# Performance work log

Measured on AMD Instinct MI355X. Metric: run time of the kernel, lower is better.

The kernel has to match this reference:

```python
import jax, jax.numpy as jnp
import numpy as np
import math

D_INNER = 512
D_STATE = 16
DT_RANK = 32
B_SZ = 2
L_SEQ = 4096


def setup_inputs() -> dict:
    key = jax.random.key(0)
    ks = jax.random.split(key, 6)
    x = jax.random.normal(ks[0], (B_SZ, L_SEQ, D_INNER), dtype=jnp.float32)
    # parameters (match torch init semantics closely enough for a numeric baseline)
    A = jnp.arange(1, D_STATE + 1, dtype=jnp.float32)
    A_log = jnp.broadcast_to(jnp.log(A)[None, :], (D_INNER, D_STATE)).copy()
    D_param = jnp.ones((D_INNER,), dtype=jnp.float32)
    # x_proj: Linear(d_inner -> dt_rank + 2*d_state), no bias
    W_xproj = jax.random.normal(ks[1], (DT_RANK + 2 * D_STATE, D_INNER), dtype=jnp.float32) / np.sqrt(D_INNER)
    # dt_proj: Linear(dt_rank -> d_inner) with special bias init
    W_dt = jax.random.normal(ks[2], (D_INNER, DT_RANK), dtype=jnp.float32) / np.sqrt(DT_RANK)
    dt_init = jnp.exp(jax.random.uniform(ks[3], (D_INNER,)) * (math.log(0.1) - math.log(0.001)) + math.log(0.001))
    b_dt = jnp.log(jnp.exp(dt_init) - 1.0)
    alpha = jnp.asarray(0.6, dtype=jnp.float32)
    beta_logit = jnp.asarray(math.log(0.99 / (1.0 - 0.99 + 1e-08)), dtype=jnp.float32)
    return {"x": x, "A_log": A_log, "D_param": D_param, "W_xproj": W_xproj,
            "W_dt": W_dt, "b_dt": b_dt, "alpha": alpha, "beta_logit": beta_logit}


def _momentum_ssm(x, A_log, D_param, W_xproj, W_dt, b_dt, alpha, beta_logit):
    # x: (B, L, D)
    proj = jnp.einsum('bld,pd->blp', x, W_xproj)            # (B, L, r+2N)
    dt_in = proj[..., :DT_RANK]
    Bp = proj[..., DT_RANK:DT_RANK + D_STATE]                # (B, L, N)
    Cp = proj[..., DT_RANK + D_STATE:]                       # (B, L, N)
    dt = jax.nn.softplus(jnp.einsum('blr,dr->bld', dt_in, W_dt) + b_dt)  # (B, L, D)
    A = -jnp.exp(A_log)                                      # (D, N)
    A_bar = jnp.exp(dt[..., None] * A[None, None])           # (B, L, D, N)
    # fused B_bar * x_t: dt * Bp * x
    inp = dt[..., None] * Bp[:, :, None, :] * x[..., None]   # (B, L, D, N)
    beta = jax.nn.sigmoid(beta_logit)

    # scan over time; carry (h, v): (B, D, N)
    h0 = jnp.zeros((x.shape[0], D_INNER, D_STATE), dtype=x.dtype)
    v0 = jnp.zeros_like(h0)

    def step(carry, ts):
        h, v = carry
        a_t, inp_t, c_t = ts                                 # (B,D,N), (B,D,N), (B,N)
        v = beta * v + alpha * inp_t
        h = a_t * h + v
        y = jnp.einsum('bdn,bn->bd', h, c_t)
        return (h, v), y

    xs = (jnp.moveaxis(A_bar, 1, 0), jnp.moveaxis(inp, 1, 0), jnp.moveaxis(Cp, 1, 0))
    _, ys = jax.lax.scan(step, (h0, v0), xs)                 # ys: (L, B, D)
    y = jnp.moveaxis(ys, 0, 1)                               # (B, L, D)
    return y + D_param * x


def reference(x, A_log, D_param, W_xproj, W_dt, b_dt, alpha, beta_logit):
    return _momentum_ssm(x, A_log, D_param, W_xproj, W_dt, b_dt, alpha, beta_logit)
```

## Files before the change

kernel.cpp:

```cpp
#include <hip/hip_runtime.h>


#define D_IN 512
#define D_ST 16
#define DTR  32
#define BSZ  2
#define LSEQ 4096
#define PDIM 64
#define NCH  256
#define LCH  (LSEQ / NCH)
#define LOG2E 1.44269504f
#define LN2   0.69314718f

typedef __attribute__((ext_vector_type(8))) short short8;
typedef __attribute__((ext_vector_type(4))) float f32x4;
typedef _Float16 f16;
typedef __attribute__((ext_vector_type(8))) _Float16 f16x8;

__device__ inline float fast_exp2(float x) { return __builtin_amdgcn_exp2f(x); }
__device__ inline float fast_log2(float x) { return __builtin_amdgcn_logf(x); }

__device__ inline unsigned short bf16_rne(float f) {
  unsigned b = __float_as_uint(f);
  return (unsigned short)((b + 0x7fffu + ((b >> 16) & 1u)) >> 16);
}

__device__ inline void cvt8(const float4 u, const float4 v, short8& hi, short8& lo) {
  float f[8] = {u.x, u.y, u.z, u.w, v.x, v.y, v.z, v.w};
#pragma unroll
  for (int i = 0; i < 8; ++i) {
    unsigned short h = bf16_rne(f[i]);
    hi[i] = (short)h;
    float r = f[i] - __uint_as_float((unsigned)h << 16);
    lo[i] = (short)bf16_rne(r);
  }
}

__device__ inline void st16h(f16* p, const float* s) {
  f16 t[16];
#pragma unroll
  for (int i = 0; i < 16; ++i) t[i] = (f16)s[i];
  *(f16x8*)p = *(f16x8*)&t[0];
  *(f16x8*)(p + 8) = *(f16x8*)&t[8];
}
__device__ inline void ld16h(const f16* p, float* d) {
  f16x8 a = *(const f16x8*)p;
  f16x8 b = *(const f16x8*)(p + 8);
#pragma unroll
  for (int i = 0; i < 8; ++i) { d[i] = (float)a[i]; d[8 + i] = (float)b[i]; }
}

#define PWCHK(val, n)                                                        \
  pw = pw && (fabsf((val) - (float)((n) + 1) * a0) <=                        \
              2e-5f * fabsf((float)((n) + 1) * a0));

__device__ inline bool detectA2(const float* __restrict__ A_log, int d, float& a0) {
  const float4* ap = (const float4*)(A_log + (size_t)d * D_ST);
  float4 r0 = ap[0], r1 = ap[1], r2 = ap[2], r3 = ap[3];
  float4 e0 = make_float4(-__expf(r0.x) * LOG2E, -__expf(r0.y) * LOG2E,
                          -__expf(r0.z) * LOG2E, -__expf(r0.w) * LOG2E);
  float4 e1 = make_float4(-__expf(r1.x) * LOG2E, -__expf(r1.y) * LOG2E,
                          -__expf(r1.z) * LOG2E, -__expf(r1.w) * LOG2E);
  float4 e2 = make_float4(-__expf(r2.x) * LOG2E, -__expf(r2.y) * LOG2E,
                          -__expf(r2.z) * LOG2E, -__expf(r2.w) * LOG2E);
  float4 e3 = make_float4(-__expf(r3.x) * LOG2E, -__expf(r3.y) * LOG2E,
                          -__expf(r3.z) * LOG2E, -__expf(r3.w) * LOG2E);
  a0 = e0.x;
  bool pw = true;
  PWCHK(e0.y, 1) PWCHK(e0.z, 2) PWCHK(e0.w, 3)
  PWCHK(e1.x, 4) PWCHK(e1.y, 5) PWCHK(e1.z, 6) PWCHK(e1.w, 7)
  PWCHK(e2.x, 8) PWCHK(e2.y, 9) PWCHK(e2.z, 10) PWCHK(e2.w, 11)
  PWCHK(e3.x, 12) PWCHK(e3.y, 13) PWCHK(e3.z, 14) PWCHK(e3.w, 15)
  return pw;
}

#define MM3(ACC, AH, AL, BH, BL)                                        \
  ACC = __builtin_amdgcn_mfma_f32_16x16x32_bf16(AL, BH, ACC, 0, 0, 0);  \
  ACC = __builtin_amdgcn_mfma_f32_16x16x32_bf16(AH, BL, ACC, 0, 0, 0);  \
  ACC = __builtin_amdgcn_mfma_f32_16x16x32_bf16(AH, BH, ACC, 0, 0, 0);

#define LOADBF(P, S)                                          \
  {                                                           \
    const int kb = (S) * 32;                                  \
    float4 a0 = *(const float4*)(wr + kb);                    \
    float4 b0 = *(const float4*)(wr + kb + 4);                \
    float4 a1 = *(const float4*)(wr + 8192 + kb);             \
    float4 b1 = *(const float4*)(wr + 8192 + kb + 4);         \
    float4 a2 = *(const float4*)(wr + 16384 + kb);            \
    float4 b2 = *(const float4*)(wr + 16384 + kb + 4);        \
    float4 a3 = *(const float4*)(wr + 24576 + kb);            \
    float4 b3 = *(const float4*)(wr + 24576 + kb + 4);        \
    cvt8(a0, b0, P##h0, P##l0);                               \
    cvt8(a1, b1, P##h1, P##l1);                               \
    cvt8(a2, b2, P##h2, P##l2);                               \
    cvt8(a3, b3, P##h3, P##l3);                               \
  }

#define LOADA(Aa, Ab, S)                              \
  {                                                   \
    const int ka = (S) * 32;                          \
    Aa = *(const float4*)(xr + ka);                   \
    Ab = *(const float4*)(xr + ka + 4);               \
  }

#define COMPSTEP(Aa, Ab, P)                           \
  {                                                   \
    short8 ahi, alo;                                  \
    cvt8(Aa, Ab, ahi, alo);                           \
    MM3(acc0, ahi, alo, P##h0, P##l0);                \
    MM3(acc1, ahi, alo, P##h1, P##l1);                \
    MM3(acc2, ahi, alo, P##h2, P##l2);                \
    MM3(acc3, ahi, alo, P##h3, P##l3);                \
  }

__global__ __launch_bounds__(256) void k_proj(const float* __restrict__ x,
                                              const float* __restrict__ W,
                                              float* __restrict__ proj) {
  __shared__ float Pacc[4][16][64];
  const int row0 = blockIdx.x * 16;
  const int l = threadIdx.x & 63;
  const int wq = threadIdx.x >> 6;
  const int m = l & 15;
  const int ko = (l >> 4) * 8 + wq * 128;
  const float* xr = x + (size_t)(row0 + m) * D_IN + ko;
  const float* wr = W + (size_t)m * D_IN + ko;

  f32x4 acc0 = {0.f, 0.f, 0.f, 0.f}, acc1 = acc0, acc2 = acc0, acc3 = acc0;
  float4 A0a, A0b, A1a, A1b, A2a, A2b, A3a, A3b;
  short8 Xh0, Xh1, Xh2, Xh3, Xl0, Xl1, Xl2, Xl3;
  short8 Yh0, Yh1, Yh2, Yh3, Yl0, Yl1, Yl2, Yl3;
  LOADA(A0a, A0b, 0); LOADA(A1a, A1b, 1); LOADA(A2a, A2b, 2); LOADA(A3a, A3b, 3);
  LOADBF(X, 0); LOADBF(Y, 1);

  COMPSTEP(A0a, A0b, X); LOADBF(X, 2);
  COMPSTEP(A1a, A1b, Y); LOADBF(Y, 3);
  COMPSTEP(A2a, A2b, X);
  COMPSTEP(A3a, A3b, Y);

  const int r0 = (l >> 4) * 4;
#pragma unroll
  for (int r = 0; r < 4; ++r) {
    Pacc[wq][r0 + r][m] = acc0[r];
    Pacc[wq][r0 + r][16 + m] = acc1[r];
    Pacc[wq][r0 + r][32 + m] = acc2[r];
    Pacc[wq][r0 + r][48 + m] = acc3[r];
  }
  __syncthreads();

  const int orow = threadIdx.x >> 4;
  const int ocol = (threadIdx.x & 15) * 4;
  float4 s0 = *(const float4*)&Pacc[0][orow][ocol];
  float4 s1 = *(const float4*)&Pacc[1][orow][ocol];
  float4 s2 = *(const float4*)&Pacc[2][orow][ocol];
  float4 s3 = *(const float4*)&Pacc[3][orow][ocol];
  float4 o = make_float4((s0.x + s1.x) + (s2.x + s3.x), (s0.y + s1.y) + (s2.y + s3.y),
                         (s0.z + s1.z) + (s2.z + s3.z), (s0.w + s1.w) + (s2.w + s3.w));
  *(float4*)(proj + (size_t)(row0 + orow) * PDIM + ocol) = o;
}

#define S1_LOOP                                                              \
  _Pragma("unroll")                                                          \
  for (int j = 0; j < LCH; ++j) {                                            \
    const float4* pj = (const float4*)(pb + j * PDIM);                       \
    float4 pp[8];                                                            \
    _Pragma("unroll")                                                        \
    for (int k = 0; k < 8; ++k) pp[k] = pj[k];                               \
    float c0 = bb, c1 = 0.f, c2 = 0.f, c3 = 0.f;                             \
    _Pragma("unroll")                                                        \
    for (int k = 0; k < 8; ++k) {                                            \
      c0 = fmaf(pp[k].x, w4[k].x, c0);                                       \
      c1 = fmaf(pp[k].y, w4[k].y, c1);                                       \
      c2 = fmaf(pp[k].z, w4[k].z, c2);                                       \
      c3 = fmaf(pp[k].w, w4[k].w, c3);                                       \
    }                                                                        \
    const float acc = (c0 + c1) + (c2 + c3);                                 \
    const float ee = fast_exp2(acc * LOG2E);                                 \
    const float dtc = (acc > 20.f) ? acc : LN2 * fast_log2(1.f + ee);        \
    dp[(size_t)j * D_IN] = (f16)dtc;                                         \
    sd += dtc;                                                               \
    bpow *= beta;                                                            \
    const float u = alpha * dtc * xs[j];                                     \
    float4 bq[4];                                                            \
    _Pragma("unroll")                                                        \
    for (int k = 0; k < 4; ++k) bq[k] = pj[8 + k];                           \
    const float* Bf = (const float*)bq;                                      \
    AR_INIT;                                                                 \
    _Pragma("unroll")                                                        \
    for (int n = 0; n < 16; ++n) {                                           \
      AR_STEP;                                                               \
      v[n] = fmaf(beta, v[n], u * Bf[n]);                                    \
      h[n] = fmaf(ar, h[n], v[n]);                                           \
      cv[n] = fmaf(ar, cv[n], bpow);                                         \
    }                                                                        \
  }

__global__ __launch_bounds__(256) void k_scan1(const float* __restrict__ x,
                                               const float* __restrict__ proj,
                                               const float* __restrict__ A_log,
                                               const float* __restrict__ W_dt,
                                               const float* __restrict__ b_dt,
                                               const float* __restrict__ alpha_p,
                                               const float* __restrict__ beta_p,
                                               f16* __restrict__ hh,
                                               f16* __restrict__ vh,
                                               f16* __restrict__ cvv,
                                               float* __restrict__ sdt,
                                               f16* __restrict__ dth) {
  const int c = blockIdx.x, b = blockIdx.z;
  const int d = blockIdx.y * 256 + threadIdx.x;
  const int t0 = c * LCH;
  const float* pb = proj + ((size_t)b * LSEQ + t0) * PDIM;

  float xs[LCH];
  {
    const float* xp = x + ((size_t)b * LSEQ + t0) * D_IN + d;
#pragma unroll
    for (int j = 0; j < LCH; ++j) xs[j] = xp[(size_t)j * D_IN];
  }
  float4 w4[8];
  {
    const float4* wp = (const float4*)(W_dt + (size_t)d * DTR);
#pragma unroll
    for (int i = 0; i < 8; ++i) w4[i] = wp[i];
  }
  const float bb = b_dt[d];
  const float alpha = alpha_p[0];
  const float beta = 1.f / (1.f + __expf(-beta_p[0]));
  float a0;
  const bool pw = detectA2(A_log, d, a0);

  f16* dp = dth + ((size_t)b * LSEQ + t0) * D_IN + d;
  float h[16] = {}, v[16] = {}, cv[16] = {};
  float bpow = 1.f, sd = 0.f;

  if (pw) {
#define AR_INIT const float r = fast_exp2(dtc * a0); float ar = 1.f
#define AR_STEP ar *= r
    S1_LOOP
#undef AR_INIT
#undef AR_STEP
  } else {
    volatile const float* av = A_log + (size_t)d * D_ST;
#define AR_INIT float ar
#define AR_STEP ar = fast_exp2(dtc * (-__expf(av[n]) * LOG2E))
    S1_LOOP
#undef AR_INIT
#undef AR_STEP
  }

  const size_t base = ((size_t)(b * NCH + c) * D_IN + d) * D_ST;
  st16h(hh + base, h);
  st16h(vh + base, v);
  st16h(cvv + base, cv);
  sdt[(size_t)(b * NCH + c) * D_IN + d] = sd;
}

__global__ __launch_bounds__(1024) void k_fix(f16* __restrict__ hh,
                                              f16* __restrict__ vh,
                                              const f16* __restrict__ cvv,
                                              const float* __restrict__ sdt,
                                              const float* __restrict__ A_log,
                                              const float* __restrict__ beta_p) {
  __shared__ float M[16][5][64];
  const int lane = threadIdx.x & 63;
  const int w = threadIdx.x >> 6;
  const int g = blockIdx.x * 64 + lane;
  const int b = g >> 13;
  const int dn = g & 8191;
  const float beta = 1.f / (1.f + __expf(-beta_p[0]));
  const float A2 = -__expf(A_log[dn]) * LOG2E;
  float bL = beta;
#pragma unroll
  for (int i = 0; i < 4; ++i) bL *= bL;

  const size_t cs = (size_t)D_IN * D_ST;
  const size_t base = (size_t)b * NCH * cs + dn;
  const size_t sbase = (size_t)b * NCH * D_IN + (dn >> 4);
  const int c0 = w * 16;

  float hc[16], vc[16], cvc[16], Pa[16];
#pragma unroll
  for (int i = 0; i < 16; ++i) {
    const int c = c0 + i;
    hc[i] = (float)hh[base + (size_t)c * cs];
    vc[i] = (float)vh[base + (size_t)c * cs];
    cvc[i] = (float)cvv[base + (size_t)c * cs];
    Pa[i] = fast_exp2(sdt[sbase + (size_t)c * D_IN] * A2);
  }
  float SP = 1.f, Sq = 0.f, Sh = 0.f, Sv = 0.f, Sw = 1.f;
#pragma unroll
  for (int i = 0; i < 16; ++i) {
    Sq = fmaf(Pa[i], Sq, cvc[i] * Sw);
    Sh = fmaf(Pa[i], Sh, fmaf(cvc[i], Sv, hc[i]));
    SP = Pa[i] * SP;
    Sv = fmaf(bL, Sv, vc[i]);
    Sw = bL * Sw;
  }
  M[w][0][lane] = SP; M[w][1][lane] = Sq; M[w][2][lane] = Sh;
  M[w][3][lane] = Sv; M[w][4][lane] = Sw;
  __syncthreads();

  float H = 0.f, V = 0.f;
  for (int s = 0; s < w; ++s) {
    const float P = M[s][0][lane], q = M[s][1][lane], h = M[s][2][lane];
    const float vv = M[s][3][lane], ww = M[s][4][lane];
    const float Hn = fmaf(P, H, fmaf(q, V, h));
    V = fmaf(ww, V, vv);
    H = Hn;
  }

#pragma unroll
  for (int i = 0; i < 16; ++i) {
    const int c = c0 + i;
    hh[base + (size_t)c * cs] = (f16)H;
    vh[base + (size_t)c * cs] = (f16)V;
    const float Hn = fmaf(Pa[i], H, fmaf(cvc[i], V, hc[i]));
    V = fmaf(bL, V, vc[i]);
    H = Hn;
  }
}

#define S2_LOOP                                                              \
  _Pragma("unroll")                                                          \
  for (int j = 0; j < LCH; ++j) {                                            \
    const float4* pj = (const float4*)(pb + j * PDIM);                       \
    float4 bq[8];                                                            \
    _Pragma("unroll")                                                        \
    for (int k = 0; k < 8; ++k) bq[k] = pj[8 + k];                           \
    const float* Bf = (const float*)bq;                                      \
    const float dtc = dtv[j], xv = xs[j];                                    \
    const float u = alpha * dtc * xv;                                        \
    float y0 = 0.f, y1 = 0.f, y2 = 0.f, y3 = 0.f;                            \
    AR_INIT;                                                                 \
    _Pragma("unroll")                                                        \
    for (int n = 0; n < 16; ++n) {                                           \
      AR_STEP;                                                               \
      v[n] = fmaf(beta, v[n], u * Bf[n]);                                    \
      h[n] = fmaf(ar, h[n], v[n]);                                           \
      float hc = h[n] * Bf[16 + n];                                          \
      if ((n & 3) == 0) y0 += hc;                                            \
      else if ((n & 3) == 1) y1 += hc;                                       \
      else if ((n & 3) == 2) y2 += hc;                                       \
      else y3 += hc;                                                         \
    }                                                                        \
    op[(size_t)j * D_IN] = (y0 + y1) + (y2 + y3) + Dv * xv;                  \
  }

__global__ __launch_bounds__(256) void k_scan2(const float* __restrict__ x,
                                               const f16* __restrict__ dth,
                                               const float* __restrict__ proj,
                                               const float* __restrict__ A_log,
                                               const float* __restrict__ D_param,
                                               const float* __restrict__ alpha_p,
                                               const float* __restrict__ beta_p,
                                               const f16* __restrict__ hh,
                                               const f16* __restrict__ vh,
                                               float* __restrict__ out) {
  const int c = blockIdx.x, b = blockIdx.z;
  const int d = blockIdx.y * 256 + threadIdx.x;
  const int t0 = c * LCH;
  const float* pb = proj + ((size_t)b * LSEQ + t0) * PDIM;

  float xs[LCH], dtv[LCH];
  {
    const float* xp = x + ((size_t)b * LSEQ + t0) * D_IN + d;
    const f16* dp = dth + ((size_t)b * LSEQ + t0) * D_IN + d;
#pragma unroll
    for (int j = 0; j < LCH; ++j) xs[j] = xp[(size_t)j * D_IN];
#pragma unroll
    for (int j = 0; j < LCH; ++j) dtv[j] = (float)dp[(size_t)j * D_IN];
  }
  const float alpha = alpha_p[0];
  const float beta = 1.f / (1.f + __expf(-beta_p[0]));
  const float Dv = D_param[d];
  float a0;
  const bool pw = detectA2(A_log, d, a0);
  const size_t ibase = ((size_t)(b * NCH + c) * D_IN + d) * D_ST;
  float h[16], v[16];
  ld16h(hh + ibase, h);
  ld16h(vh + ibase, v);

  float* op = out + ((size_t)b * LSEQ + t0) * D_IN + d;
  if (pw) {
#define AR_INIT const float r = fast_exp2(dtc * a0); float ar = 1.f
#define AR_STEP ar *= r
    S2_LOOP
#undef AR_INIT
#undef AR_STEP
  } else {
    volatile const float* av = A_log + (size_t)d * D_ST;
#define AR_INIT float ar
#define AR_STEP ar = fast_exp2(dtc * (-__expf(av[n]) * LOG2E))
    S2_LOOP
#undef AR_INIT
#undef AR_STEP
  }
}

extern "C" void kernel_launch(void* const* d_in, const int* in_sizes, int n_in,
                              void* d_out, int out_size, void* d_ws, size_t ws_size,
                              hipStream_t stream) {
  const float* x = (const float*)d_in[0];
  const float* A_log = (const float*)d_in[1];
  const float* D_param = (const float*)d_in[2];
  const float* W_xproj = (const float*)d_in[3];
  const float* W_dt = (const float*)d_in[4];
  const float* b_dt = (const float*)d_in[5];
  const float* alpha = (const float*)d_in[6];
  const float* beta_logit = (const float*)d_in[7];
  float* out = (float*)d_out;

  const size_t NST = (size_t)BSZ * NCH * D_IN * D_ST;
  float* ws = (float*)d_ws;
  float* proj = ws;
  float* sdt = proj + (size_t)BSZ * LSEQ * PDIM;
  f16* hh = (f16*)(sdt + (size_t)BSZ * NCH * D_IN);
  f16* vh = hh + NST;
  f16* cvv = vh + NST;
  f16* dth = cvv + NST;

  k_proj<<<dim3(BSZ * LSEQ / 16), dim3(256), 0, stream>>>(x, W_xproj, proj);
  k_scan1<<<dim3(NCH, D_IN / 256, BSZ), dim3(256), 0, stream>>>(
      x, proj, A_log, W_dt, b_dt, alpha, beta_logit, hh, vh, cvv, sdt, dth);
  k_fix<<<dim3(BSZ * D_IN * D_ST / 64), dim3(1024), 0, stream>>>(hh, vh, cvv, sdt,
                                                                 A_log, beta_logit);
  k_scan2<<<dim3(NCH, D_IN / 256, BSZ), dim3(256), 0, stream>>>(
      x, dth, proj, A_log, D_param, alpha, beta_logit, hh, vh, out);
}
```

Before: 156.5 us.

## Double scan chunk count and pack fix-pass state as half pairs

Raises the number of time chunks from 256 to 512, which halves the chunk length used by the chunked scan stages and gives the sequential stages more parallelism. The fix kernel now covers 32 chunks per wave. To keep register use down, it stores the per-chunk h, v and cv values as packed 16-bit pairs and recomputes the decay factor in the second pass instead of keeping it. The cost is twice as much chunk-boundary state traffic and a longer sequential combine in the fix kernel.

```diff
diff --git a/kernel.cpp b/kernel.cpp
--- a/kernel.cpp
+++ b/kernel.cpp
@@ -7,8 +7,10 @@
 #define BSZ  2
 #define LSEQ 4096
 #define PDIM 64
-#define NCH  256
+#define NCH  512
 #define LCH  (LSEQ / NCH)
+#define LOG2LCH 3
+#define CPS  32
 #define LOG2E 1.44269504f
 #define LN2   0.69314718f
 
@@ -23,6 +25,12 @@
 __device__ inline unsigned short bf16_rne(float f) {
   unsigned b = __float_as_uint(f);
   return (unsigned short)((b + 0x7fffu + ((b >> 16) & 1u)) >> 16);
+}
+
+__device__ inline float h2f(unsigned short u) {
+  f16 t;
+  __builtin_memcpy(&t, &u, 2);
+  return (float)t;
 }
 
 __device__ inline void cvt8(const float4 u, const float4 v, short8& hi, short8& lo) {
@@ -271,29 +279,34 @@
   const float A2 = -__expf(A_log[dn]) * LOG2E;
   float bL = beta;
 #pragma unroll
-  for (int i = 0; i < 4; ++i) bL *= bL;
+  for (int i = 0; i < LOG2LCH; ++i) bL *= bL;
 
   const size_t cs = (size_t)D_IN * D_ST;
   const size_t base = (size_t)b * NCH * cs + dn;
   const size_t sbase = (size_t)b * NCH * D_IN + (dn >> 4);
-  const int c0 = w * 16;
-
-  float hc[16], vc[16], cvc[16], Pa[16];
-#pragma unroll
-  for (int i = 0; i < 16; ++i) {
+  const int c0 = w * CPS;
+
+  unsigned hr[CPS / 2], vr[CPS / 2], cr[CPS / 2];
+  float SP = 1.f, Sq = 0.f, Sh = 0.f, Sv = 0.f, Sw = 1.f;
+#pragma unroll
+  for (int i = 0; i < CPS; ++i) {
     const int c = c0 + i;
-    hc[i] = (float)hh[base + (size_t)c * cs];
-    vc[i] = (float)vh[base + (size_t)c * cs];
-    cvc[i] = (float)cvv[base + (size_t)c * cs];
-    Pa[i] = fast_exp2(sdt[sbase + (size_t)c * D_IN] * A2);
-  }
-  float SP = 1.f, Sq = 0.f, Sh = 0.f, Sv = 0.f, Sw = 1.f;
-#pragma unroll
-  for (int i = 0; i < 16; ++i) {
-    Sq = fmaf(Pa[i], Sq, cvc[i] * Sw);
-    Sh = fmaf(Pa[i], Sh, fmaf(cvc[i], Sv, hc[i]));
-    SP = Pa[i] * SP;
-    Sv = fmaf(bL, Sv, vc[i]);
+    const unsigned short hu = *(const unsigned short*)(hh + base + (size_t)c * cs);
+    const unsigned short vu = *(const unsigned short*)(vh + base + (size_t)c * cs);
+    const unsigned short cu = *(const unsigned short*)(cvv + base + (size_t)c * cs);
+    if ((i & 1) == 0) {
+      hr[i / 2] = hu; vr[i / 2] = vu; cr[i / 2] = cu;
+    } else {
+      hr[i / 2] |= (unsigned)hu << 16;
+      vr[i / 2] |= (unsigned)vu << 16;
+      cr[i / 2] |= (unsigned)cu << 16;
+    }
+    const float hc = h2f(hu), vc = h2f(vu), cvc = h2f(cu);
+    const float Pa = fast_exp2(sdt[sbase + (size_t)c * D_IN] * A2);
+    Sq = fmaf(Pa, Sq, cvc * Sw);
+    Sh = fmaf(Pa, Sh, fmaf(cvc, Sv, hc));
+    SP = Pa * SP;
+    Sv = fmaf(bL, Sv, vc);
     Sw = bL * Sw;
   }
   M[w][0][lane] = SP; M[w][1][lane] = Sq; M[w][2][lane] = Sh;
@@ -310,12 +323,19 @@
   }
 
 #pragma unroll
-  for (int i = 0; i < 16; ++i) {
+  for (int i = 0; i < CPS; ++i) {
     const int c = c0 + i;
+    const unsigned short hu =
+        (i & 1) ? (unsigned short)(hr[i / 2] >> 16) : (unsigned short)(hr[i / 2] & 0xffffu);
+    const unsigned short vu =
+        (i & 1) ? (unsigned short)(vr[i / 2] >> 16) : (unsigned short)(vr[i / 2] & 0xffffu);
+    const unsigned short cu =
+        (i & 1) ? (unsigned short)(cr[i / 2] >> 16) : (unsigned short)(cr[i / 2] & 0xffffu);
+    const float Pa = fast_exp2(sdt[sbase + (size_t)c * D_IN] * A2);
     hh[base + (size_t)c * cs] = (f16)H;
     vh[base + (size_t)c * cs] = (f16)V;
-    const float Hn = fmaf(Pa[i], H, fmaf(cvc[i], V, hc[i]));
-    V = fmaf(bL, V, vc[i]);
+    const float Hn = fmaf(Pa, H, fmaf(h2f(cu), V, h2f(hu)));
+    V = fmaf(bL, V, h2f(vu));
     H = Hn;
   }
 }
```

New measurement: 188.8 us. +20.6%, slower.

## Split scan1 state dimension across two lanes per channel

Applied to the files above, without the earlier changes.

The first chunked scan pass now gives each channel two threads, each handling 8 of the 16 state entries and half of the dt_rank dot product, combined with a lane shuffle. This doubles the thread count and halves per-thread register use (h, v, cv arrays and weights), which is meant to raise occupancy and parallelism in k_scan1. x is now loaded one step ahead instead of all at once. In exchange, the softplus and exp are computed redundantly in both lanes and proj reads are partly duplicated.

```diff
diff --git a/kernel.cpp b/kernel.cpp
--- a/kernel.cpp
+++ b/kernel.cpp
@@ -36,12 +36,11 @@
   }
 }
 
-__device__ inline void st16h(f16* p, const float* s) {
-  f16 t[16];
-#pragma unroll
-  for (int i = 0; i < 16; ++i) t[i] = (f16)s[i];
+__device__ inline void st8h(f16* p, const float* s) {
+  f16 t[8];
+#pragma unroll
+  for (int i = 0; i < 8; ++i) t[i] = (f16)s[i];
   *(f16x8*)p = *(f16x8*)&t[0];
-  *(f16x8*)(p + 8) = *(f16x8*)&t[8];
 }
 __device__ inline void ld16h(const f16* p, float* d) {
   f16x8 a = *(const f16x8*)p;
@@ -158,39 +157,39 @@
   *(float4*)(proj + (size_t)(row0 + orow) * PDIM + ocol) = o;
 }
 
-#define S1_LOOP                                                              \
+#define S1P_LOOP                                                             \
   _Pragma("unroll")                                                          \
   for (int j = 0; j < LCH; ++j) {                                            \
-    const float4* pj = (const float4*)(pb + j * PDIM);                       \
-    float4 pp[8];                                                            \
+    const float xv = xc;                                                     \
+    if (j < LCH - 1) xc = xp[(size_t)(j + 1) * D_IN];                        \
+    const float* pj = pb + j * PDIM + 16 * hf;                               \
+    float c0 = 0.f, c1 = 0.f, c2 = 0.f, c3 = 0.f;                            \
     _Pragma("unroll")                                                        \
-    for (int k = 0; k < 8; ++k) pp[k] = pj[k];                               \
-    float c0 = bb, c1 = 0.f, c2 = 0.f, c3 = 0.f;                             \
+    for (int k = 0; k < 4; ++k) {                                            \
+      float4 p = ((const float4*)pj)[k];                                     \
+      c0 = fmaf(p.x, w4[k].x, c0);                                           \
+      c1 = fmaf(p.y, w4[k].y, c1);                                           \
+      c2 = fmaf(p.z, w4[k].z, c2);                                           \
+      c3 = fmaf(p.w, w4[k].w, c3);                                           \
+    }                                                                        \
+    const float part = (c0 + c1) + (c2 + c3);                                \
+    const float acc = part + __shfl_xor(part, 1, 64) + bb;                   \
+    const float ee = fast_exp2(acc * LOG2E);                                 \
+    const float dtc = (acc > 20.f) ? acc : LN2 * fast_log2(1.f + ee);        \
+    if (hf == 0) dp[(size_t)j * D_IN] = (f16)dtc;                            \
+    sd += dtc;                                                               \
+    bpow *= beta;                                                            \
+    const float u = alpha * dtc * xv;                                        \
+    float4 B0 = *(const float4*)(pb + j * PDIM + DTR + 8 * hf);              \
+    float4 B1 = *(const float4*)(pb + j * PDIM + DTR + 8 * hf + 4);          \
+    const float Bf[8] = {B0.x, B0.y, B0.z, B0.w, B1.x, B1.y, B1.z, B1.w};    \
+    AR_INIT;                                                                 \
     _Pragma("unroll")                                                        \
     for (int k = 0; k < 8; ++k) {                                            \
-      c0 = fmaf(pp[k].x, w4[k].x, c0);                                       \
-      c1 = fmaf(pp[k].y, w4[k].y, c1);                                       \
-      c2 = fmaf(pp[k].z, w4[k].z, c2);                                       \
-      c3 = fmaf(pp[k].w, w4[k].w, c3);                                       \
-    }                                                                        \
-    const float acc = (c0 + c1) + (c2 + c3);                                 \
-    const float ee = fast_exp2(acc * LOG2E);                                 \
-    const float dtc = (acc > 20.f) ? acc : LN2 * fast_log2(1.f + ee);        \
-    dp[(size_t)j * D_IN] = (f16)dtc;                                         \
-    sd += dtc;                                                               \
-    bpow *= beta;                                                            \
-    const float u = alpha * dtc * xs[j];                                     \
-    float4 bq[4];                                                            \
-    _Pragma("unroll")                                                        \
-    for (int k = 0; k < 4; ++k) bq[k] = pj[8 + k];                           \
-    const float* Bf = (const float*)bq;                                      \
-    AR_INIT;                                                                 \
-    _Pragma("unroll")                                                        \
-    for (int n = 0; n < 16; ++n) {                                           \
       AR_STEP;                                                               \
-      v[n] = fmaf(beta, v[n], u * Bf[n]);                                    \
-      h[n] = fmaf(ar, h[n], v[n]);                                           \
-      cv[n] = fmaf(ar, cv[n], bpow);                                         \
+      v8[k] = fmaf(beta, v8[k], u * Bf[k]);                                  \
+      h8[k] = fmaf(ar, h8[k], v8[k]);                                        \
+      cv8[k] = fmaf(ar, cv8[k], bpow);                                       \
     }                                                                        \
   }
 
@@ -207,52 +206,58 @@
                                                float* __restrict__ sdt,
                                                f16* __restrict__ dth) {
   const int c = blockIdx.x, b = blockIdx.z;
-  const int d = blockIdx.y * 256 + threadIdx.x;
+  const int hf = threadIdx.x & 1;
+  const int d = blockIdx.y * 128 + (threadIdx.x >> 1);
   const int t0 = c * LCH;
   const float* pb = proj + ((size_t)b * LSEQ + t0) * PDIM;
 
-  float xs[LCH];
+  float a0;
+  const bool pw = detectA2(A_log, d, a0);
+
+  float4 w4[4];
   {
-    const float* xp = x + ((size_t)b * LSEQ + t0) * D_IN + d;
-#pragma unroll
-    for (int j = 0; j < LCH; ++j) xs[j] = xp[(size_t)j * D_IN];
-  }
-  float4 w4[8];
-  {
-    const float4* wp = (const float4*)(W_dt + (size_t)d * DTR);
-#pragma unroll
-    for (int i = 0; i < 8; ++i) w4[i] = wp[i];
+    const float4* wp = (const float4*)(W_dt + (size_t)d * DTR + 16 * hf);
+#pragma unroll
+    for (int i = 0; i < 4; ++i) w4[i] = wp[i];
   }
   const float bb = b_dt[d];
   const float alpha = alpha_p[0];
   const float beta = 1.f / (1.f + __expf(-beta_p[0]));
-  float a0;
-  const bool pw = detectA2(A_log, d, a0);
-
+
+  const float* xp = x + ((size_t)b * LSEQ + t0) * D_IN + d;
   f16* dp = dth + ((size_t)b * LSEQ + t0) * D_IN + d;
-  float h[16] = {}, v[16] = {}, cv[16] = {};
+  float xc = xp[0];
+
+  float h8[8] = {}, v8[8] = {}, cv8[8] = {};
   float bpow = 1.f, sd = 0.f;
 
   if (pw) {
-#define AR_INIT const float r = fast_exp2(dtc * a0); float ar = 1.f
+#define AR_INIT                                                   \
+    const float r = fast_exp2(dtc * a0);                          \
+    float ar;                                                     \
+    {                                                             \
+      const float r2 = r * r;                                     \
+      const float r4 = r2 * r2;                                   \
+      ar = hf ? r4 * r4 : 1.f;                                    \
+    }
 #define AR_STEP ar *= r
-    S1_LOOP
+    S1P_LOOP
 #undef AR_INIT
 #undef AR_STEP
   } else {
-    volatile const float* av = A_log + (size_t)d * D_ST;
+    volatile const float* av = A_log + (size_t)d * D_ST + 8 * hf;
 #define AR_INIT float ar
-#define AR_STEP ar = fast_exp2(dtc * (-__expf(av[n]) * LOG2E))
-    S1_LOOP
+#define AR_STEP ar = fast_exp2(dtc * (-__expf(av[k]) * LOG2E))
+    S1P_LOOP
 #undef AR_INIT
 #undef AR_STEP
   }
 
-  const size_t base = ((size_t)(b * NCH + c) * D_IN + d) * D_ST;
-  st16h(hh + base, h);
-  st16h(vh + base, v);
-  st16h(cvv + base, cv);
-  sdt[(size_t)(b * NCH + c) * D_IN + d] = sd;
+  const size_t base = ((size_t)(b * NCH + c) * D_IN + d) * D_ST + hf * 8;
+  st8h(hh + base, h8);
+  st8h(vh + base, v8);
+  st8h(cvv + base, cv8);
+  if (hf == 0) sdt[(size_t)(b * NCH + c) * D_IN + d] = sd;
 }
 
 __global__ __launch_bounds__(1024) void k_fix(f16* __restrict__ hh,
@@ -420,7 +425,7 @@
   f16* dth = cvv + NST;
 
   k_proj<<<dim3(BSZ * LSEQ / 16), dim3(256), 0, stream>>>(x, W_xproj, proj);
-  k_scan1<<<dim3(NCH, D_IN / 256, BSZ), dim3(256), 0, stream>>>(
+  k_scan1<<<dim3(NCH, D_IN / 128, BSZ), dim3(256), 0, stream>>>(
       x, proj, A_log, W_dt, b_dt, alpha, beta_logit, hh, vh, cvv, sdt, dth);
   k_fix<<<dim3(BSZ * D_IN * D_ST / 64), dim3(1024), 0, stream>>>(hh, vh, cvv, sdt,
                                                                  A_log, beta_logit);
```

Measured after the change: 187.0 us. +19.5%, slower.
